# Performance work log

Measured on AMD Instinct MI355X. Metric: run time of the kernel, lower is better.

Reference implementation:

```python
import jax, jax.numpy as jnp
import numpy as np

B, C, IC, H, W = 16, 2048, 1024, 32, 32  # note: H*W must equal IC (quirk of original code)
BN_EPS = 1e-5


def conv1x1(x, w, b):
    # x: (B,C,H,W), w: (O,C), b: (O,)
    return jnp.einsum('oc,bchw->bohw', w, x) + b[None, :, None, None]


def setup_inputs() -> dict:
    key = jax.random.key(0)
    ks = jax.random.split(key, 9)
    s = lambda k, shape, scale=0.02: jax.random.normal(k, shape, jnp.float32) * scale
    return {
        'x_this': jax.random.normal(ks[0], (B, C, H, W), jnp.float32),
        'x_other': jax.random.normal(ks[1], (B, C, H, W), jnp.float32),
        'g_w': s(ks[2], (IC, C)), 'g_b': jnp.zeros((IC,), jnp.float32),
        'theta_w': s(ks[3], (IC, C)), 'theta_b': jnp.zeros((IC,), jnp.float32),
        'phi_w': s(ks[4], (IC, C)), 'phi_b': jnp.zeros((IC,), jnp.float32),
        'wz_w': s(ks[5], (C, IC)), 'wz_b': jnp.zeros((C,), jnp.float32),
        'bn_gamma': s(ks[6], (C,), 0.1), 'bn_beta': s(ks[7], (C,), 0.1),
    }


def reference(x_this, x_other, g_w, g_b, theta_w, theta_b, phi_w, phi_b,
              wz_w, wz_b, bn_gamma, bn_beta):
    b, c, h, w = x_this.shape
    ic = g_w.shape[0]
    hw = h * w  # == ic by construction (required by the original code's matmul)
    g_x = conv1x1(x_this, g_w, g_b).reshape(b, ic, hw)          # (B,IC,HW)
    theta_x = conv1x1(x_this, theta_w, theta_b).reshape(b, ic, hw)
    phi_x = conv1x1(x_other, phi_w, phi_b).reshape(b, ic, hw)
    # f = phi_x^T-free: matmul(phi_x, theta_x^T) per original: (B,HW,HW)
    f = jnp.einsum('bci,bcj->bij', phi_x, theta_x)
    f_div_C = jax.nn.softmax(f, axis=-1)
    # original (buggy but faithful) matmul: (B,HW,HW) @ (B,IC,HW) with HW==IC
    y = jnp.matmul(f_div_C, g_x)                                # (B,HW,HW)
    y = y.reshape(b, ic, h, w)
    wy = conv1x1(y, wz_w, wz_b)                                  # (B,C,H,W)
    # BatchNorm2d in training mode: batch statistics over (N,H,W)
    mean = wy.mean(axis=(0, 2, 3))
    var = wy.var(axis=(0, 2, 3))
    wy = (wy - mean[None, :, None, None]) * jax.lax.rsqrt(var[None, :, None, None] + BN_EPS)
    wy = wy * bn_gamma[None, :, None, None] + bn_beta[None, :, None, None]
    return wy + x_this
```

## Files before the change

kernel.cpp:

```cpp
#include <hip/hip_runtime.h>


typedef __attribute__((ext_vector_type(4))) float f32x4;
typedef __attribute__((ext_vector_type(8))) short bf16x8;

__device__ __forceinline__ float bf2f(unsigned s16) {
  union { unsigned u; float f; } v; v.u = s16 << 16; return v.f;
}
__device__ __forceinline__ unsigned short f2bf(float f) {
  union { float f; unsigned u; } v; v.f = f;
  unsigned r = v.u + 0x7FFFu + ((v.u >> 16) & 1u);
  return (unsigned short)(r >> 16);
}

__device__ __forceinline__ void gload_lds16(const unsigned short* g, unsigned short* l) {
  __builtin_amdgcn_global_load_lds((const __attribute__((address_space(1))) void*)g,
                                   (__attribute__((address_space(3))) void*)l, 16, 0, 0);
}

#define SWAIT_VM8()   asm volatile("s_waitcnt vmcnt(8)" ::: "memory")
#define SWAIT_VM0()   asm volatile("s_waitcnt vmcnt(0)" ::: "memory")
#define SWAIT_LGKM0() asm volatile("s_waitcnt lgkmcnt(0)" ::: "memory")
#define SCHED_BAR()   __builtin_amdgcn_sched_barrier(0)
#define SBAR()        __builtin_amdgcn_s_barrier()

template<int OUT_F32, int BIAS_MODE>
__global__ __launch_bounds__(256, 2)
void mm_bt(const unsigned short* __restrict__ A, const unsigned short* __restrict__ Bt,
           void* __restrict__ Cv, const float* __restrict__ bias,
           int N, int K, long sA, long sB, long sC, int nbx, int nby)
{
  __shared__ __align__(16) unsigned short lds[32768];
  const int tid = threadIdx.x;
  const int wave = tid >> 6, lane = tid & 63;

  const int nwg = nbx * nby * 16;
  const int cpx = nwg >> 3;
  const int swz = (blockIdx.x & 7) * cpx + (blockIdx.x >> 3);
  const int bx = swz % nbx;
  const int rem = swz / nbx;
  const int by = rem % nby;
  const long z = rem / nby;
  const int bm = by * 128, bn = bx * 128;

  const unsigned short* Ab = A + z * sA;
  const unsigned short* Bb = Bt + z * sB;

  long gAo[4], gBo[4];
  int  lEo[4];
#pragma unroll
  for (int s = 0; s < 4; ++s) {
    const int q = s * 256 + tid;
    const int row = q >> 3, sl = q & 7;
    const int gsl = sl ^ (row & 7);
    gAo[s] = (long)(bm + row) * K + gsl * 8;
    gBo[s] = (long)(bn + row) * K + gsl * 8;
    lEo[s] = q * 8;
  }

  const int wr = wave >> 1, wc = wave & 1;
  const int l15 = lane & 15, kgl = lane >> 4;
  int aoff[2][4], boff[2][4];
#pragma unroll
  for (int kk = 0; kk < 2; ++kk)
#pragma unroll
    for (int m = 0; m < 4; ++m) {
      const int ra = wr * 64 + m * 16 + l15;
      aoff[kk][m] = ra * 64 + ((kk * 4 + kgl) ^ (ra & 7)) * 8;
      const int rb = wc * 64 + m * 16 + l15;
      boff[kk][m] = 8192 + rb * 64 + ((kk * 4 + kgl) ^ (rb & 7)) * 8;
    }

  const int NT = K >> 6;

  {
    unsigned short* l0 = &lds[0];
#pragma unroll
    for (int s = 0; s < 4; ++s) gload_lds16(Ab + gAo[s], l0 + lEo[s]);
#pragma unroll
    for (int s = 0; s < 4; ++s) gload_lds16(Bb + gBo[s], l0 + 8192 + lEo[s]);
    unsigned short* l1 = &lds[16384];
#pragma unroll
    for (int s = 0; s < 4; ++s) gload_lds16(Ab + gAo[s] + 64, l1 + lEo[s]);
#pragma unroll
    for (int s = 0; s < 4; ++s) gload_lds16(Bb + gBo[s] + 64, l1 + 8192 + lEo[s]);
  }
  SWAIT_VM8(); SCHED_BAR();
  SBAR();

  f32x4 acc[4][4];
#pragma unroll
  for (int i = 0; i < 4; ++i)
#pragma unroll
    for (int j = 0; j < 4; ++j) acc[i][j] = (f32x4)0.f;

  for (int t = 0; t < NT; ++t) {
    const int bufo = (t & 1) * 16384;
    bf16x8 af[2][4], bg[2][4];
#pragma unroll
    for (int kk = 0; kk < 2; ++kk)
#pragma unroll
      for (int m = 0; m < 4; ++m) {
        af[kk][m] = *(const bf16x8*)&lds[bufo + aoff[kk][m]];
        bg[kk][m] = *(const bf16x8*)&lds[bufo + boff[kk][m]];
      }
    SWAIT_LGKM0(); SCHED_BAR();
    SBAR();
    SCHED_BAR();
    if (t + 2 < NT) {
      const long kb = (long)(t + 2) * 64;
      unsigned short* lb = &lds[bufo];
#pragma unroll
      for (int s = 0; s < 4; ++s) gload_lds16(Ab + gAo[s] + kb, lb + lEo[s]);
#pragma unroll
      for (int s = 0; s < 4; ++s) gload_lds16(Bb + gBo[s] + kb, lb + 8192 + lEo[s]);
    }
    __builtin_amdgcn_s_setprio(1);
#pragma unroll
    for (int kk = 0; kk < 2; ++kk)
#pragma unroll
      for (int m = 0; m < 4; ++m)
#pragma unroll
        for (int n = 0; n < 4; ++n)
          acc[m][n] = __builtin_amdgcn_mfma_f32_16x16x32_bf16(af[kk][m], bg[kk][n], acc[m][n], 0, 0, 0);
    __builtin_amdgcn_s_setprio(0);
    if (t + 2 < NT) { SWAIT_VM8(); } else { SWAIT_VM0(); }
    SCHED_BAR();
    SBAR();
  }

  const int col0 = bn + wc * 64 + l15;
  const int row0 = bm + wr * 64 + (lane >> 4) * 4;
#pragma unroll
  for (int m = 0; m < 4; ++m) {
#pragma unroll
    for (int n = 0; n < 4; ++n) {
      const int cc = col0 + n * 16;
      float bcol = (BIAS_MODE == 2) ? bias[cc] : 0.0f;
#pragma unroll
      for (int r = 0; r < 4; ++r) {
        const int rr = row0 + m * 16 + r;
        float v = acc[m][n][r] + ((BIAS_MODE == 1) ? bias[rr] : bcol);
        if (OUT_F32) ((float*)Cv)[z * sC + (long)rr * N + cc] = v;
        else ((unsigned short*)Cv)[z * sC + (long)rr * N + cc] = f2bf(v);
      }
    }
  }
}

__global__ __launch_bounds__(256)
void tr_bf_k(const float* __restrict__ in, unsigned short* __restrict__ out, int R, int CC)
{
  __shared__ float t[32][33];
  const long z = blockIdx.z;
  const int r0 = blockIdx.y * 32, c0 = blockIdx.x * 32;
  const float* ip = in + z * (long)R * CC;
  unsigned short* op = out + z * (long)R * CC;
  const int tx = threadIdx.x & 31, ty = threadIdx.x >> 5;
#pragma unroll
  for (int i = 0; i < 32; i += 8)
    t[ty + i][tx] = ip[(long)(r0 + ty + i) * CC + c0 + tx];
  __syncthreads();
  const int oc = threadIdx.x >> 3;
  const int orr = (threadIdx.x & 7) * 4;
  ushort4 o;
  o.x = f2bf(t[orr + 0][oc]); o.y = f2bf(t[orr + 1][oc]);
  o.z = f2bf(t[orr + 2][oc]); o.w = f2bf(t[orr + 3][oc]);
  *(ushort4*)&op[(long)(c0 + oc) * R + r0 + orr] = o;
}

__global__ void w2bf_k(const float* __restrict__ w0, const float* __restrict__ w1,
                       const float* __restrict__ w2, const float* __restrict__ w3,
                       unsigned short* __restrict__ out)
{
  long g = blockIdx.x * (long)blockDim.x + threadIdx.x;
  const long st = (long)gridDim.x * blockDim.x;
  for (; g < 2097152; g += st) {
    const int seg = (int)(g >> 19);
    const long loc = g & 524287;
    const float* src = (seg == 0) ? w0 : (seg == 1) ? w1 : (seg == 2) ? w2 : w3;
    float4 v = *(const float4*)(src + loc * 4);
    ushort4 o; o.x = f2bf(v.x); o.y = f2bf(v.y); o.z = f2bf(v.z); o.w = f2bf(v.w);
    *(ushort4*)(out + g * 4) = o;
  }
}

__global__ __launch_bounds__(256)
void softmax_k(const float* __restrict__ f, unsigned short* __restrict__ P)
{
  const long row = blockIdx.x;
  const float* fr = f + row * 1024;
  unsigned short* pr = P + row * 1024;
  const int tid = threadIdx.x;
  const int lane = tid & 63, wid = tid >> 6;
  float v[4];
  float mx = -1e30f;
#pragma unroll
  for (int i = 0; i < 4; ++i) { v[i] = fr[tid + i * 256]; mx = fmaxf(mx, v[i]); }
  for (int o = 32; o; o >>= 1) mx = fmaxf(mx, __shfl_xor(mx, o));
  __shared__ float redm[4];
  if (!lane) redm[wid] = mx;
  __syncthreads();
  mx = fmaxf(fmaxf(redm[0], redm[1]), fmaxf(redm[2], redm[3]));
  float s = 0.f;
#pragma unroll
  for (int i = 0; i < 4; ++i) { v[i] = __expf(v[i] - mx); s += v[i]; }
  for (int o = 32; o; o >>= 1) s += __shfl_xor(s, o);
  __shared__ float reds[4];
  if (!lane) reds[wid] = s;
  __syncthreads();
  s = reds[0] + reds[1] + reds[2] + reds[3];
  const float inv = 1.0f / s;
#pragma unroll
  for (int i = 0; i < 4; ++i) pr[tid + i * 256] = f2bf(v[i] * inv);
}

__global__ __launch_bounds__(256)
void bn_stats_k(const unsigned short* __restrict__ wy, float* __restrict__ stats)
{
  const int c = blockIdx.x;
  const int tid = threadIdx.x;
  const int lane = tid & 63, wid = tid >> 6;
  float s = 0.f, ss = 0.f;
  for (int b = 0; b < 16; ++b) {
    const unsigned short* p = wy + ((long)b * 2048 + c) * 1024 + tid * 4;
    uint2 u = *(const uint2*)p;
    float v0 = bf2f(u.x & 0xFFFFu), v1 = bf2f(u.x >> 16);
    float v2 = bf2f(u.y & 0xFFFFu), v3 = bf2f(u.y >> 16);
    s += v0 + v1 + v2 + v3;
    ss += v0 * v0 + v1 * v1 + v2 * v2 + v3 * v3;
  }
  for (int o = 32; o; o >>= 1) { s += __shfl_xor(s, o); ss += __shfl_xor(ss, o); }
  __shared__ float rs[4], rss[4];
  if (!lane) { rs[wid] = s; rss[wid] = ss; }
  __syncthreads();
  if (tid == 0) {
    s = rs[0] + rs[1] + rs[2] + rs[3];
    ss = rss[0] + rss[1] + rss[2] + rss[3];
    const float mean = s * (1.0f / 16384.0f);
    const float var = ss * (1.0f / 16384.0f) - mean * mean;
    stats[2 * c] = mean;
    stats[2 * c + 1] = rsqrtf(var + 1e-5f);
  }
}

__global__ void bn_final_k(const unsigned short* __restrict__ wy,
                           const float* __restrict__ x_this,
                           const float* __restrict__ stats,
                           const float* __restrict__ gamma,
                           const float* __restrict__ beta,
                           float* __restrict__ out, long n4)
{
  long i = blockIdx.x * (long)blockDim.x + threadIdx.x;
  const long st = (long)gridDim.x * blockDim.x;
  for (; i < n4; i += st) {
    const long e = i * 4;
    const int c = (int)((e >> 10) & 2047);
    const float mean = stats[2 * c], rstd = stats[2 * c + 1];
    const float ga = gamma[c] * rstd;
    const float be = beta[c] - mean * ga;
    uint2 u = *(const uint2*)(wy + e);
    float4 x = *(const float4*)(x_this + e);
    float4 o;
    o.x = bf2f(u.x & 0xFFFFu) * ga + be + x.x;
    o.y = bf2f(u.x >> 16)     * ga + be + x.y;
    o.z = bf2f(u.y & 0xFFFFu) * ga + be + x.z;
    o.w = bf2f(u.y >> 16)     * ga + be + x.w;
    *(float4*)(out + e) = o;
  }
}

extern "C" void kernel_launch(void* const* d_in, const int* in_sizes, int n_in,
                              void* d_out, int out_size, void* d_ws, size_t ws_size,
                              hipStream_t stream) {
  const float* x_this  = (const float*)d_in[0];
  const float* x_other = (const float*)d_in[1];
  const float* g_w     = (const float*)d_in[2];
  const float* g_b     = (const float*)d_in[3];
  const float* theta_w = (const float*)d_in[4];
  const float* theta_b = (const float*)d_in[5];
  const float* phi_w   = (const float*)d_in[6];
  const float* phi_b   = (const float*)d_in[7];
  const float* wz_w    = (const float*)d_in[8];
  const float* wz_b    = (const float*)d_in[9];
  const float* bn_gamma= (const float*)d_in[10];
  const float* bn_beta = (const float*)d_in[11];
  float* out = (float*)d_out;
  char* ws = (char*)d_ws;
  const size_t MB = 1ull << 20;

  unsigned short* wg  = (unsigned short*)(ws + 0 * MB);
  unsigned short* wth = (unsigned short*)(ws + 4 * MB);
  unsigned short* wph = (unsigned short*)(ws + 8 * MB);
  unsigned short* wwz = (unsigned short*)(ws + 12 * MB);
  unsigned short* xtT = (unsigned short*)(ws + 16 * MB);
  unsigned short* xoT = (unsigned short*)(ws + 80 * MB);
  unsigned short* gT  = (unsigned short*)(ws + 144 * MB);
  unsigned short* thT = (unsigned short*)(ws + 176 * MB);
  unsigned short* phT = (unsigned short*)(ws + 208 * MB);
  float*          fb  = (float*)         (ws + 16 * MB);
  unsigned short* P   = (unsigned short*)(ws + 80 * MB);
  unsigned short* yT  = (unsigned short*)(ws + 112 * MB);
  unsigned short* wy  = (unsigned short*)(ws + 176 * MB);
  float*          st  = (float*)         (ws + 240 * MB);

  const long S1M = 1l << 20;
  const long S2M = 2l << 20;

  w2bf_k<<<dim3(2048), dim3(256), 0, stream>>>(g_w, theta_w, phi_w, wz_w, wg);
  tr_bf_k<<<dim3(32, 64, 16), dim3(256), 0, stream>>>(x_this,  xtT, 2048, 1024);
  tr_bf_k<<<dim3(32, 64, 16), dim3(256), 0, stream>>>(x_other, xoT, 2048, 1024);

  mm_bt<0, 2><<<dim3(1024), dim3(256), 0, stream>>>(xtT, wg,  gT,  g_b,     1024, 2048, S2M, 0, S1M, 8, 8);
  mm_bt<0, 2><<<dim3(1024), dim3(256), 0, stream>>>(xtT, wth, thT, theta_b, 1024, 2048, S2M, 0, S1M, 8, 8);
  mm_bt<0, 2><<<dim3(1024), dim3(256), 0, stream>>>(xoT, wph, phT, phi_b,   1024, 2048, S2M, 0, S1M, 8, 8);
  mm_bt<1, 0><<<dim3(1024), dim3(256), 0, stream>>>(phT, thT, fb, nullptr, 1024, 1024, S1M, S1M, S1M, 8, 8);
  softmax_k<<<dim3(16384), dim3(256), 0, stream>>>(fb, P);
  mm_bt<0, 0><<<dim3(1024), dim3(256), 0, stream>>>(gT, P, yT, nullptr, 1024, 1024, S1M, S1M, S1M, 8, 8);
  mm_bt<0, 1><<<dim3(2048), dim3(256), 0, stream>>>(wwz, yT, wy, wz_b, 1024, 1024, 0, S1M, S2M, 8, 16);
  bn_stats_k<<<dim3(2048), dim3(256), 0, stream>>>(wy, st);
  bn_final_k<<<dim3(4096), dim3(256), 0, stream>>>(wy, x_this, st, bn_gamma, bn_beta, out, 33554432 / 4);
  (void)ws_size; (void)n_in; (void)in_sizes; (void)out_size;
  (void)wth; (void)wph;
}
```

Measured before the change: 810.5 us.

## Enlarge GEMM tiles to 256x256 with 8 waves and staged fragment loads

```diff
diff --git a/kernel.cpp b/kernel.cpp
--- a/kernel.cpp
+++ b/kernel.cpp
@@ -23,14 +23,15 @@
 #define SWAIT_LGKM0() asm volatile("s_waitcnt lgkmcnt(0)" ::: "memory")
 #define SCHED_BAR()   __builtin_amdgcn_sched_barrier(0)
 #define SBAR()        __builtin_amdgcn_s_barrier()
+#define MFMA16(a, b, c) __builtin_amdgcn_mfma_f32_16x16x32_bf16(a, b, c, 0, 0, 0)
 
 template<int OUT_F32, int BIAS_MODE>
-__global__ __launch_bounds__(256, 2)
+__global__ __launch_bounds__(512, 2)
 void mm_bt(const unsigned short* __restrict__ A, const unsigned short* __restrict__ Bt,
            void* __restrict__ Cv, const float* __restrict__ bias,
            int N, int K, long sA, long sB, long sC, int nbx, int nby)
 {
-  __shared__ __align__(16) unsigned short lds[32768];
+  __shared__ __align__(16) unsigned short lds[65536];
   const int tid = threadIdx.x;
   const int wave = tid >> 6, lane = tid & 63;
 
@@ -41,98 +42,123 @@
   const int rem = swz / nbx;
   const int by = rem % nby;
   const long z = rem / nby;
-  const int bm = by * 128, bn = bx * 128;
+  const int bm = by * 256, bn = bx * 256;
 
   const unsigned short* Ab = A + z * sA;
   const unsigned short* Bb = Bt + z * sB;
 
-  long gAo[4], gBo[4];
-  int  lEo[4];
-#pragma unroll
-  for (int s = 0; s < 4; ++s) {
-    const int q = s * 256 + tid;
+  int gAo[4], gBo[4], lEo[4];
+#pragma unroll
+  for (int j = 0; j < 4; ++j) {
+    const int q = j * 512 + tid;
     const int row = q >> 3, sl = q & 7;
     const int gsl = sl ^ (row & 7);
-    gAo[s] = (long)(bm + row) * K + gsl * 8;
-    gBo[s] = (long)(bn + row) * K + gsl * 8;
-    lEo[s] = q * 8;
-  }
-
-  const int wr = wave >> 1, wc = wave & 1;
+    gAo[j] = (bm + row) * K + gsl * 8;
+    gBo[j] = (bn + row) * K + gsl * 8;
+    lEo[j] = q * 8;
+  }
+
+  const int wr = wave >> 2, wc = wave & 3;
   const int l15 = lane & 15, kgl = lane >> 4;
-  int aoff[2][4], boff[2][4];
-#pragma unroll
-  for (int kk = 0; kk < 2; ++kk)
-#pragma unroll
-    for (int m = 0; m < 4; ++m) {
-      const int ra = wr * 64 + m * 16 + l15;
-      aoff[kk][m] = ra * 64 + ((kk * 4 + kgl) ^ (ra & 7)) * 8;
-      const int rb = wc * 64 + m * 16 + l15;
-      boff[kk][m] = 8192 + rb * 64 + ((kk * 4 + kgl) ^ (rb & 7)) * 8;
-    }
+  int aoff[8], boff[4];
+#pragma unroll
+  for (int m = 0; m < 8; ++m) {
+    const int ra = wr * 128 + m * 16 + l15;
+    aoff[m] = ra * 64 + (kgl ^ (ra & 7)) * 8;
+  }
+#pragma unroll
+  for (int n = 0; n < 4; ++n) {
+    const int rb = wc * 64 + n * 16 + l15;
+    boff[n] = 16384 + rb * 64 + (kgl ^ (rb & 7)) * 8;
+  }
 
   const int NT = K >> 6;
 
   {
-    unsigned short* l0 = &lds[0];
-#pragma unroll
-    for (int s = 0; s < 4; ++s) gload_lds16(Ab + gAo[s], l0 + lEo[s]);
-#pragma unroll
-    for (int s = 0; s < 4; ++s) gload_lds16(Bb + gBo[s], l0 + 8192 + lEo[s]);
-    unsigned short* l1 = &lds[16384];
-#pragma unroll
-    for (int s = 0; s < 4; ++s) gload_lds16(Ab + gAo[s] + 64, l1 + lEo[s]);
-#pragma unroll
-    for (int s = 0; s < 4; ++s) gload_lds16(Bb + gBo[s] + 64, l1 + 8192 + lEo[s]);
+#pragma unroll
+    for (int j = 0; j < 4; ++j) gload_lds16(Ab + gAo[j], &lds[lEo[j]]);
+#pragma unroll
+    for (int j = 0; j < 4; ++j) gload_lds16(Bb + gBo[j], &lds[16384 + lEo[j]]);
+#pragma unroll
+    for (int j = 0; j < 4; ++j) gload_lds16(Ab + gAo[j] + 64, &lds[32768 + lEo[j]]);
+#pragma unroll
+    for (int j = 0; j < 4; ++j) gload_lds16(Bb + gBo[j] + 64, &lds[32768 + 16384 + lEo[j]]);
   }
   SWAIT_VM8(); SCHED_BAR();
   SBAR();
 
-  f32x4 acc[4][4];
-#pragma unroll
-  for (int i = 0; i < 4; ++i)
+  f32x4 acc[8][4];
+#pragma unroll
+  for (int i = 0; i < 8; ++i)
 #pragma unroll
     for (int j = 0; j < 4; ++j) acc[i][j] = (f32x4)0.f;
 
   for (int t = 0; t < NT; ++t) {
-    const int bufo = (t & 1) * 16384;
-    bf16x8 af[2][4], bg[2][4];
-#pragma unroll
-    for (int kk = 0; kk < 2; ++kk)
-#pragma unroll
-      for (int m = 0; m < 4; ++m) {
-        af[kk][m] = *(const bf16x8*)&lds[bufo + aoff[kk][m]];
-        bg[kk][m] = *(const bf16x8*)&lds[bufo + boff[kk][m]];
-      }
+    const int bufo = (t & 1) * 32768;
+    bf16x8 af[8], b0, b1;
+#pragma unroll
+    for (int m = 0; m < 8; ++m) af[m] = *(const bf16x8*)&lds[bufo + aoff[m]];
+    b0 = *(const bf16x8*)&lds[bufo + boff[0]];
+    b1 = *(const bf16x8*)&lds[bufo + boff[1]];
     SWAIT_LGKM0(); SCHED_BAR();
+    __builtin_amdgcn_s_setprio(1);
+#pragma unroll
+    for (int m = 0; m < 8; ++m) {
+      acc[m][0] = MFMA16(af[m], b0, acc[m][0]);
+      acc[m][1] = MFMA16(af[m], b1, acc[m][1]);
+    }
+    __builtin_amdgcn_s_setprio(0);
+    b0 = *(const bf16x8*)&lds[bufo + boff[2]];
+    b1 = *(const bf16x8*)&lds[bufo + boff[3]];
+    SWAIT_LGKM0(); SCHED_BAR();
+    __builtin_amdgcn_s_setprio(1);
+#pragma unroll
+    for (int m = 0; m < 8; ++m) {
+      acc[m][2] = MFMA16(af[m], b0, acc[m][2]);
+      acc[m][3] = MFMA16(af[m], b1, acc[m][3]);
+    }
+    __builtin_amdgcn_s_setprio(0);
+#pragma unroll
+    for (int m = 0; m < 8; ++m) af[m] = *(const bf16x8*)&lds[bufo + (aoff[m] ^ 32)];
+    b0 = *(const bf16x8*)&lds[bufo + (boff[0] ^ 32)];
+    b1 = *(const bf16x8*)&lds[bufo + (boff[1] ^ 32)];
+    SWAIT_LGKM0(); SCHED_BAR();
+    __builtin_amdgcn_s_setprio(1);
+#pragma unroll
+    for (int m = 0; m < 8; ++m) {
+      acc[m][0] = MFMA16(af[m], b0, acc[m][0]);
+      acc[m][1] = MFMA16(af[m], b1, acc[m][1]);
+    }
+    __builtin_amdgcn_s_setprio(0);
+    b0 = *(const bf16x8*)&lds[bufo + (boff[2] ^ 32)];
+    b1 = *(const bf16x8*)&lds[bufo + (boff[3] ^ 32)];
+    SWAIT_LGKM0(); SCHED_BAR();
+    __builtin_amdgcn_s_setprio(1);
+#pragma unroll
+    for (int m = 0; m < 8; ++m) {
+      acc[m][2] = MFMA16(af[m], b0, acc[m][2]);
+      acc[m][3] = MFMA16(af[m], b1, acc[m][3]);
+    }
+    __builtin_amdgcn_s_setprio(0);
     SBAR();
-    SCHED_BAR();
     if (t + 2 < NT) {
       const long kb = (long)(t + 2) * 64;
-      unsigned short* lb = &lds[bufo];
-#pragma unroll
-      for (int s = 0; s < 4; ++s) gload_lds16(Ab + gAo[s] + kb, lb + lEo[s]);
-#pragma unroll
-      for (int s = 0; s < 4; ++s) gload_lds16(Bb + gBo[s] + kb, lb + 8192 + lEo[s]);
-    }
-    __builtin_amdgcn_s_setprio(1);
-#pragma unroll
-    for (int kk = 0; kk < 2; ++kk)
-#pragma unroll
-      for (int m = 0; m < 4; ++m)
-#pragma unroll
-        for (int n = 0; n < 4; ++n)
-          acc[m][n] = __builtin_amdgcn_mfma_f32_16x16x32_bf16(af[kk][m], bg[kk][n], acc[m][n], 0, 0, 0);
-    __builtin_amdgcn_s_setprio(0);
-    if (t + 2 < NT) { SWAIT_VM8(); } else { SWAIT_VM0(); }
+#pragma unroll
+      for (int j = 0; j < 4; ++j) gload_lds16(Ab + gAo[j] + kb, &lds[bufo + lEo[j]]);
+#pragma unroll
+      for (int j = 0; j < 4; ++j) gload_lds16(Bb + gBo[j] + kb, &lds[bufo + 16384 + lEo[j]]);
+      SWAIT_VM8();
+    } else {
+      SWAIT_VM0();
+    }
     SCHED_BAR();
     SBAR();
   }
 
   const int col0 = bn + wc * 64 + l15;
-  const int row0 = bm + wr * 64 + (lane >> 4) * 4;
-#pragma unroll
-  for (int m = 0; m < 4; ++m) {
+  const int row0 = bm + wr * 128 + (lane >> 4) * 4;
+#pragma unroll
+  for (int m = 0; m < 8; ++m) {
 #pragma unroll
     for (int n = 0; n < 4; ++n) {
       const int cc = col0 + n * 16;
@@ -311,13 +337,13 @@
   tr_bf_k<<<dim3(32, 64, 16), dim3(256), 0, stream>>>(x_this,  xtT, 2048, 1024);
   tr_bf_k<<<dim3(32, 64, 16), dim3(256), 0, stream>>>(x_other, xoT, 2048, 1024);
 
-  mm_bt<0, 2><<<dim3(1024), dim3(256), 0, stream>>>(xtT, wg,  gT,  g_b,     1024, 2048, S2M, 0, S1M, 8, 8);
-  mm_bt<0, 2><<<dim3(1024), dim3(256), 0, stream>>>(xtT, wth, thT, theta_b, 1024, 2048, S2M, 0, S1M, 8, 8);
-  mm_bt<0, 2><<<dim3(1024), dim3(256), 0, stream>>>(xoT, wph, phT, phi_b,   1024, 2048, S2M, 0, S1M, 8, 8);
-  mm_bt<1, 0><<<dim3(1024), dim3(256), 0, stream>>>(phT, thT, fb, nullptr, 1024, 1024, S1M, S1M, S1M, 8, 8);
+  mm_bt<0, 2><<<dim3(256), dim3(512), 0, stream>>>(xtT, wg,  gT,  g_b,     1024, 2048, S2M, 0, S1M, 4, 4);
+  mm_bt<0, 2><<<dim3(256), dim3(512), 0, stream>>>(xtT, wth, thT, theta_b, 1024, 2048, S2M, 0, S1M, 4, 4);
+  mm_bt<0, 2><<<dim3(256), dim3(512), 0, stream>>>(xoT, wph, phT, phi_b,   1024, 2048, S2M, 0, S1M, 4, 4);
+  mm_bt<1, 0><<<dim3(256), dim3(512), 0, stream>>>(phT, thT, fb, nullptr, 1024, 1024, S1M, S1M, S1M, 4, 4);
   softmax_k<<<dim3(16384), dim3(256), 0, stream>>>(fb, P);
-  mm_bt<0, 0><<<dim3(1024), dim3(256), 0, stream>>>(gT, P, yT, nullptr, 1024, 1024, S1M, S1M, S1M, 8, 8);
-  mm_bt<0, 1><<<dim3(2048), dim3(256), 0, stream>>>(wwz, yT, wy, wz_b, 1024, 1024, 0, S1M, S2M, 8, 16);
+  mm_bt<0, 0><<<dim3(256), dim3(512), 0, stream>>>(gT, P, yT, nullptr, 1024, 1024, S1M, S1M, S1M, 4, 4);
+  mm_bt<0, 1><<<dim3(512), dim3(512), 0, stream>>>(wwz, yT, wy, wz_b, 1024, 1024, 0, S1M, S2M, 4, 8);
   bn_stats_k<<<dim3(2048), dim3(256), 0, stream>>>(wy, st);
   bn_final_k<<<dim3(4096), dim3(256), 0, stream>>>(wy, x_this, st, bn_gamma, bn_beta, out, 33554432 / 4);
   (void)ws_size; (void)n_in; (void)in_sizes; (void)out_size;
```

Result: no change. 808.5 us (-0.3%).
